# Optimization experiments

Hardware: AMD Instinct MI355X
Metric: run time of the kernel (lower is better)

The kernel has to match this reference:

```python
import jax, jax.numpy as jnp
import numpy as np

SR = 48000.0
STAB_EPS = 1e-3
BS = 32
N_FRAMES = 128
N_SAMPLES = 65536


def setup_inputs() -> dict:
    key = jax.random.key(0)
    ks = jax.random.split(key, 8)
    f0_hz = jax.random.uniform(ks[0], (BS,), minval=50.0, maxval=500.0)
    note_on_duration = jax.random.uniform(ks[1], (BS,), minval=0.3, maxval=1.0)
    phase = jax.random.uniform(ks[2], (BS,), minval=-np.pi, maxval=np.pi)
    logits = jax.random.normal(ks[3], (BS, N_FRAMES, 5))
    osc_shape = jax.random.uniform(ks[4], (BS,))
    osc_gain = jax.random.uniform(ks[5], (BS,), minval=0.5, maxval=1.0)
    dist_gain = jax.random.uniform(ks[6], (BS,), minval=1.0, maxval=4.0)
    learned_alpha = jax.random.uniform(ks[7], (BS,), minval=0.5, maxval=3.0)
    return dict(f0_hz=f0_hz, note_on_duration=note_on_duration, phase=phase,
                logits=logits, osc_shape=osc_shape, osc_gain=osc_gain,
                dist_gain=dist_gain, learned_alpha=learned_alpha,
                n_samples=N_SAMPLES)


def lin_interp_dim1(x, n_out):
    """Linear interpolation along dim 1 with align_corners=True. x: (bs, n_in, c)."""
    n_in = x.shape[1]
    pos = jnp.linspace(0.0, n_in - 1.0, n_out)
    i0 = jnp.floor(pos).astype(jnp.int32)
    i1 = jnp.minimum(i0 + 1, n_in - 1)
    frac = (pos - i0.astype(x.dtype))[None, :, None]
    return x[:, i0] * (1.0 - frac) + x[:, i1] * frac


def square_saw_vco(f0_hz, osc_shape, n_samples, phase):
    """torchsynth-style square/saw morph oscillator. f0_hz, osc_shape, phase: (bs,)."""
    f0 = f0_hz[:, None]                                   # (bs, 1)
    inc = jnp.broadcast_to(f0 / SR, (f0.shape[0], n_samples))
    arg = 2.0 * jnp.pi * jnp.cumsum(inc, axis=1) + phase[:, None]
    partials = 12000.0 / (f0 * jnp.log10(f0))
    square = jnp.tanh(jnp.pi * partials * jnp.sin(arg) / 2.0)
    s = osc_shape[:, None]
    return (1.0 - s / 2.0) * square * (1.0 + s * jnp.cos(arg / 2.0))


def exp_decay_env(alpha, note_on_duration, n_samples):
    t = jnp.arange(n_samples, dtype=jnp.float32) / SR     # (n,)
    ramp = jnp.clip(1.0 - t[None, :] / note_on_duration[:, None], STAB_EPS, 1.0)
    env = ramp ** alpha[:, None]
    return jnp.where(t[None, :] <= note_on_duration[:, None], env, 0.0)


def logits_to_a_coeff_triangle(a_logits):
    """Map 2 logits to a stable biquad denominator (a1, a2) inside the stability triangle."""
    stab = 1.0 - STAB_EPS
    a1 = 2.0 * jnp.tanh(a_logits[..., 0]) * stab
    a1_abs = jnp.abs(a1)
    a2 = ((2.0 - a1_abs) * jnp.tanh(a_logits[..., 1]) * stab + a1_abs) / 2.0
    return jnp.stack([a1, a2], axis=-1)


def sample_wise_lpc(x, a):
    """Time-varying all-pole order-2: y[t] = x[t] - a1[t]*y[t-1] - a2[t]*y[t-2].
    x: (bs, n), a: (bs, n, 2). Sequential lax.scan over time."""
    def step(carry, inp):
        y1, y2 = carry
        xt, a1, a2 = inp
        y = xt - a1 * y1 - a2 * y2
        return (y, y1), y
    z = jnp.zeros(x.shape[0], dtype=x.dtype)
    xs = (x.T, a[..., 0].T, a[..., 1].T)                  # time-major
    _, ys = jax.lax.scan(step, (z, z), xs)
    return ys.T


def time_varying_fir(x, b):
    """y[t] = b0[t]*x[t] + b1[t]*x[t-1] + b2[t]*x[t-2], zero initial state."""
    x1 = jnp.pad(x, ((0, 0), (1, 0)))[:, :-1]
    x2 = jnp.pad(x, ((0, 0), (2, 0)))[:, :-2]
    return b[..., 0] * x + b[..., 1] * x1 + b[..., 2] * x2


def reference(f0_hz, note_on_duration, phase, logits, osc_shape, osc_gain,
              dist_gain, learned_alpha, n_samples):
    # --- oscillator + envelope ---
    dry = square_saw_vco(f0_hz, osc_shape, n_samples, phase)
    dry = dry * osc_gain[:, None]
    envelope = exp_decay_env(learned_alpha, note_on_duration, n_samples)
    dry = dry * envelope
    # --- coefficients (interp_logits=False: map to coeffs at frame rate, then upsample) ---
    a_coeff = logits_to_a_coeff_triangle(logits[..., :2])   # (bs, n_frames, 2)
    b_coeff = logits[..., 2:]                                # (bs, n_frames, 3)
    a_coeff = lin_interp_dim1(a_coeff, n_samples)            # (bs, n, 2)
    b_coeff = lin_interp_dim1(b_coeff, n_samples)            # (bs, n, 3)
    # --- time-varying biquad: all-pole recursion then FIR ---
    y_a = sample_wise_lpc(dry, a_coeff)
    y_ab = time_varying_fir(y_a, b_coeff)
    # --- distortion ---
    wet = jnp.tanh(y_ab * dist_gain[:, None])
    a0 = jnp.ones_like(a_coeff[:, :, 0])
    a_coeff3 = jnp.stack([a0, a_coeff[:, :, 0], a_coeff[:, :, 1]], axis=2)
    return (dry, wet, envelope, y_ab, a_coeff3, b_coeff, y_a)
```

## Files before the change

### kernel.cpp

```cpp
#include <hip/hip_runtime.h>
#include <cmath>

#define DI __device__ __forceinline__

constexpr int BS = 32;
constexpr int NS = 65536;
constexpr int NF = 128;
constexpr int S  = 4;
constexpr int TB = 256;
constexpr int SAMP = TB * S;
constexpr int NC = NS / SAMP;
constexpr size_t U = (size_t)BS * NS;
constexpr double PI_D = 3.14159265358979323846;
constexpr float STAB = 0.999f;

struct M6 { float a, b, c, d, u, v; };

DI M6 comp(const M6& R, const M6& L) {
    M6 o;
    o.a = fmaf(R.a, L.a, R.b * L.c);
    o.b = fmaf(R.a, L.b, R.b * L.d);
    o.c = fmaf(R.c, L.a, R.d * L.c);
    o.d = fmaf(R.c, L.b, R.d * L.d);
    o.u = fmaf(R.a, L.u, fmaf(R.b, L.v, R.u));
    o.v = fmaf(R.c, L.u, fmaf(R.d, L.v, R.v));
    return o;
}

DI void stepL(M6& A, float a1, float a2, float x) {
    float na = fmaf(-a1, A.a, -a2 * A.c);
    float nb = fmaf(-a1, A.b, -a2 * A.d);
    float nu = fmaf(-a1, A.u, fmaf(-a2, A.v, x));
    A.c = A.a; A.d = A.b; A.v = A.u;
    A.a = na;  A.b = nb;  A.u = nu;
}

DI void wave_scan6(M6& s, int lane) {
    #pragma unroll
    for (int d = 1; d < 64; d <<= 1) {
        M6 o;
        o.a = __shfl_up(s.a, d, 64); o.b = __shfl_up(s.b, d, 64);
        o.c = __shfl_up(s.c, d, 64); o.d = __shfl_up(s.d, d, 64);
        o.u = __shfl_up(s.u, d, 64); o.v = __shfl_up(s.v, d, 64);
        M6 t = comp(s, o);
        bool p = lane >= d;
        s.a = p ? t.a : s.a; s.b = p ? t.b : s.b; s.c = p ? t.c : s.c;
        s.d = p ? t.d : s.d; s.u = p ? t.u : s.u; s.v = p ? t.v : s.v;
    }
}

DI M6 ld6(const float* p) { M6 m; m.a=p[0]; m.b=p[1]; m.c=p[2]; m.d=p[3]; m.u=p[4]; m.v=p[5]; return m; }
DI void st6(float* p, const M6& m) { p[0]=m.a; p[1]=m.b; p[2]=m.c; p[3]=m.d; p[4]=m.u; p[5]=m.v; }

DI void ipos(int t, int& i0, int& i1, float& fr) {
    double pos = (double)t * (127.0 / 65535.0);
    int p0 = (int)pos;
    i0 = p0;
    i1 = (p0 + 1 > 127) ? 127 : p0 + 1;
    fr = (float)(pos - (double)p0);
}

DI float fast_tanh(float x) {
    float e = __expf(2.0f * x);
    return 1.0f - 2.0f / (e + 1.0f);
}

DI void stage_frames(const float* __restrict__ logits, int b, int F, int tid,
                     float (*sfa)[2], float (*sfb)[3]) {
    if (tid < 4) {
        int fidx = F + tid; if (fidx > 127) fidx = 127;
        const float* L = logits + (size_t)(b * NF + fidx) * 5;
        float a1 = 2.0f * tanhf(L[0]) * STAB;
        float aa = fabsf(a1);
        float a2 = ((2.0f - aa) * tanhf(L[1]) * STAB + aa) * 0.5f;
        sfa[tid][0] = a1; sfa[tid][1] = a2;
        sfb[tid][0] = L[2]; sfb[tid][1] = L[3]; sfb[tid][2] = L[4];
    }
}

DI void interp4(int t0, int F, const float (*sfa)[2], const float (*sfb)[3],
                float* a1v, float* a2v, float* b0v, float* b1v, float* b2v) {
    #pragma unroll
    for (int k = 0; k < S; k++) {
        int i0, i1; float fr;
        ipos(t0 + k, i0, i1, fr);
        float w0 = 1.0f - fr;
        int l0 = i0 - F, l1 = i1 - F;
        a1v[k] = sfa[l0][0] * w0 + sfa[l1][0] * fr;
        a2v[k] = sfa[l0][1] * w0 + sfa[l1][1] * fr;
        b0v[k] = sfb[l0][0] * w0 + sfb[l1][0] * fr;
        b1v[k] = sfb[l0][1] * w0 + sfb[l1][1] * fr;
        b2v[k] = sfb[l0][2] * w0 + sfb[l1][2] * fr;
    }
}

__global__ __launch_bounds__(TB) void k_osc(
    const float* __restrict__ f0_hz, const float* __restrict__ note_dur,
    const float* __restrict__ phase, const float* __restrict__ logits,
    const float* __restrict__ osc_shape, const float* __restrict__ osc_gain,
    const float* __restrict__ alpha,
    float* __restrict__ ws_chunk, float* __restrict__ out) {
    __shared__ float sfa[4][2], sfb[4][3], wt[4][6];
    const int bid = blockIdx.x;
    const int b = bid / NC, c = bid % NC;
    const int tid = threadIdx.x;
    const int t0 = c * SAMP + tid * S;
    const size_t g0 = (size_t)b * NS + t0;
    const int F = (int)((double)(c * SAMP) * (127.0 / 65535.0));

    stage_frames(logits, b, F, tid, sfa, sfb);

    const float f0 = f0_hz[b];
    const float ph = phase[b];
    const float sh = osc_shape[b];
    const float gn = osc_gain[b];
    const float dur = note_dur[b];
    const float al = alpha[b];
    const double inc = (double)f0 / 48000.0;
    const float partials = 12000.0f / (f0 * __log10f(f0));

    const double cum0 = (double)(t0 + 1) * inc;
    const double uu0 = cum0 - 2.0 * floor(cum0 * 0.5);
    const float theta0 = (float)(PI_D * uu0 + 0.5 * (double)ph);
    const float dth = (float)(PI_D * inc);

    float x[S], env4[S];
    #pragma unroll
    for (int k = 0; k < S; k++) {
        int t = t0 + k;
        float theta = theta0 + (float)k * dth;
        float sn, cs;
        __sincosf(theta, &sn, &cs);
        float sq = fast_tanh(1.57079632679f * partials * (2.0f * sn * cs));
        float dry0 = (1.0f - 0.5f * sh) * sq * (1.0f + sh * cs);
        float tsec = (float)t * (1.0f / 48000.0f);
        float env = 0.0f;
        if (tsec <= dur) {
            float ramp = 1.0f - tsec / dur;
            ramp = ramp < 0.001f ? 0.001f : (ramp > 1.0f ? 1.0f : ramp);
            env = __expf(al * __logf(ramp));
        }
        env4[k] = env;
        x[k] = dry0 * gn * env;
    }
    __syncthreads();

    float a1v[S], a2v[S], b0v[S], b1v[S], b2v[S];
    interp4(t0, F, sfa, sfb, a1v, a2v, b0v, b1v, b2v);

    *(float4*)&out[g0]         = make_float4(x[0], x[1], x[2], x[3]);
    *(float4*)&out[2 * U + g0] = make_float4(env4[0], env4[1], env4[2], env4[3]);
    float* a3 = out + 4 * U + g0 * 3;
    *(float4*)&a3[0] = make_float4(1.0f, a1v[0], a2v[0], 1.0f);
    *(float4*)&a3[4] = make_float4(a1v[1], a2v[1], 1.0f, a1v[2]);
    *(float4*)&a3[8] = make_float4(a2v[2], 1.0f, a1v[3], a2v[3]);
    float* bc = out + 7 * U + g0 * 3;
    *(float4*)&bc[0] = make_float4(b0v[0], b1v[0], b2v[0], b0v[1]);
    *(float4*)&bc[4] = make_float4(b1v[1], b2v[1], b0v[2], b1v[2]);
    *(float4*)&bc[8] = make_float4(b2v[2], b0v[3], b1v[3], b2v[3]);

    M6 A; A.a = -a1v[0]; A.b = -a2v[0]; A.c = 1.0f; A.d = 0.0f; A.u = x[0]; A.v = 0.0f;
    #pragma unroll
    for (int k = 1; k < S; k++) stepL(A, a1v[k], a2v[k], x[k]);

    const int lane = tid & 63, w = tid >> 6;
    wave_scan6(A, lane);
    if (lane == 63) st6(wt[w], A);
    __syncthreads();
    if (tid == TB - 1) {
        M6 p = ld6(wt[0]);
        p = comp(ld6(wt[1]), p);
        p = comp(ld6(wt[2]), p);
        M6 tot = comp(A, p);
        st6(ws_chunk + ((size_t)b * NC + c) * 6, tot);
    }
}

__global__ __launch_bounds__(TB) void k_iir(
    const float* __restrict__ logits, const float* __restrict__ dist_gain,
    const float* __restrict__ ws_chunk, float* __restrict__ out) {
    __shared__ float sfa[4][2], sfb[4][3], wt[4][6], sv[NC][2];
    const int bid = blockIdx.x;
    const int b = bid / NC, c = bid % NC;
    const int tid = threadIdx.x;
    const int t0 = c * SAMP + tid * S;
    const size_t g0 = (size_t)b * NS + t0;
    const int F = (int)((double)(c * SAMP) * (127.0 / 65535.0));

    stage_frames(logits, b, F, tid, sfa, sfb);

    if (tid < NC) {
        M6 cs = ld6(ws_chunk + ((size_t)b * NC + tid) * 6);
        wave_scan6(cs, tid);
        sv[tid][0] = cs.u; sv[tid][1] = cs.v;
    }

    float4 xv = *(const float4*)&out[g0];
    float x[S] = {xv.x, xv.y, xv.z, xv.w};

    __syncthreads();
    const float s0 = c ? sv[c - 1][0] : 0.0f;
    const float s1 = c ? sv[c - 1][1] : 0.0f;

    float a1v[S], a2v[S], b0v[S], b1v[S], b2v[S];
    interp4(t0, F, sfa, sfb, a1v, a2v, b0v, b1v, b2v);

    M6 A; A.a = -a1v[0]; A.b = -a2v[0]; A.c = 1.0f; A.d = 0.0f; A.u = x[0]; A.v = 0.0f;
    #pragma unroll
    for (int k = 1; k < S; k++) stepL(A, a1v[k], a2v[k], x[k]);

    const int lane = tid & 63, w = tid >> 6;
    wave_scan6(A, lane);
    if (lane == 63) st6(wt[w], A);
    __syncthreads();

    M6 P; P.a = 1.f; P.b = 0.f; P.c = 0.f; P.d = 1.f; P.u = 0.f; P.v = 0.f;
    for (int i = 0; i < w; i++) P = comp(ld6(wt[i]), P);
    M6 prev;
    prev.a = __shfl_up(A.a, 1, 64); prev.b = __shfl_up(A.b, 1, 64);
    prev.c = __shfl_up(A.c, 1, 64); prev.d = __shfl_up(A.d, 1, 64);
    prev.u = __shfl_up(A.u, 1, 64); prev.v = __shfl_up(A.v, 1, 64);
    M6 E = (lane == 0) ? P : comp(prev, P);

    float y1 = fmaf(E.a, s0, fmaf(E.b, s1, E.u));
    float y2 = fmaf(E.c, s0, fmaf(E.d, s1, E.v));
    const float ys0 = y1, ys1 = y2;

    float y[S];
    #pragma unroll
    for (int k = 0; k < S; k++) {
        y[k] = fmaf(-a1v[k], y1, fmaf(-a2v[k], y2, x[k]));
        y2 = y1; y1 = y[k];
    }

    const float dg = dist_gain[b];
    float yab[S], wet[S];
    #pragma unroll
    for (int k = 0; k < S; k++) {
        float ym1 = (k >= 1) ? y[k - 1] : ys0;
        float ym2 = (k >= 2) ? y[k - 2] : ((k == 1) ? ys0 : ys1);
        yab[k] = b0v[k] * y[k] + b1v[k] * ym1 + b2v[k] * ym2;
        wet[k] = fast_tanh(yab[k] * dg);
    }

    *(float4*)&out[U + g0]      = make_float4(wet[0], wet[1], wet[2], wet[3]);
    *(float4*)&out[3 * U + g0]  = make_float4(yab[0], yab[1], yab[2], yab[3]);
    *(float4*)&out[10 * U + g0] = make_float4(y[0], y[1], y[2], y[3]);
}

extern "C" void kernel_launch(void* const* d_in, const int* in_sizes, int n_in,
                              void* d_out, int out_size, void* d_ws, size_t ws_size,
                              hipStream_t stream) {
    const float* f0   = (const float*)d_in[0];
    const float* dur  = (const float*)d_in[1];
    const float* ph   = (const float*)d_in[2];
    const float* lg   = (const float*)d_in[3];
    const float* shp  = (const float*)d_in[4];
    const float* gn   = (const float*)d_in[5];
    const float* dist = (const float*)d_in[6];
    const float* alp  = (const float*)d_in[7];
    float* out = (float*)d_out;
    float* ws_chunk = (float*)d_ws;

    k_osc<<<BS * NC, TB, 0, stream>>>(f0, dur, ph, lg, shp, gn, alp, ws_chunk, out);
    k_iir<<<BS * NC, TB, 0, stream>>>(lg, dist, ws_chunk, out);
}
```

Measured before the change: 130.6 us.

## Fuse oscillator and IIR kernels with decoupled look-back chunk scan

Merges the two-pass oscillator and IIR kernels into one kernel that keeps the dry signal and coefficients in registers. Blocks take a dynamic ticket to order chunks, publish their chunk transfer matrix with a release flag, and wait on predecessor flags before scanning them to get the carry-in state. This removes the second kernel's re-read of dry samples, its frame staging and coefficient re-interpolation, and one launch. In exchange it adds a tiny clear kernel, spin-waiting on global flags, and a bounded-guard loop that could silently produce wrong carries if a predecessor never arrives.

```diff
diff --git a/kernel.cpp b/kernel.cpp
--- a/kernel.cpp
+++ b/kernel.cpp
@@ -10,9 +10,14 @@
 constexpr int TB = 256;
 constexpr int SAMP = TB * S;
 constexpr int NC = NS / SAMP;
+constexpr int NBLK = BS * NC;
 constexpr size_t U = (size_t)BS * NS;
 constexpr double PI_D = 3.14159265358979323846;
 constexpr float STAB = 0.999f;
+
+__device__ unsigned int g_flags[NBLK];
+__device__ unsigned int g_tick;
+__device__ float        g_chunk[NBLK * 6];
 
 struct M6 { float a, b, c, d, u, v; };
 
@@ -94,16 +99,27 @@
     }
 }
 
-__global__ __launch_bounds__(TB) void k_osc(
+__global__ __launch_bounds__(TB) void k_clear() {
+    int i = blockIdx.x * TB + threadIdx.x;
+    if (i < NBLK) g_flags[i] = 0u;
+    if (i == 0) g_tick = 0u;
+}
+
+__global__ __launch_bounds__(TB) void k_fused(
     const float* __restrict__ f0_hz, const float* __restrict__ note_dur,
     const float* __restrict__ phase, const float* __restrict__ logits,
     const float* __restrict__ osc_shape, const float* __restrict__ osc_gain,
-    const float* __restrict__ alpha,
-    float* __restrict__ ws_chunk, float* __restrict__ out) {
-    __shared__ float sfa[4][2], sfb[4][3], wt[4][6];
-    const int bid = blockIdx.x;
-    const int b = bid / NC, c = bid % NC;
+    const float* __restrict__ dist_gain, const float* __restrict__ alpha,
+    float* __restrict__ out) {
+    __shared__ float sfa[4][2], sfb[4][3], wt[4][6], sIn[2];
+    __shared__ int s_v;
     const int tid = threadIdx.x;
+
+    if (tid == 0) s_v = (int)atomicAdd(&g_tick, 1u);
+    __syncthreads();
+    const int v = s_v;
+    const int b = v & (BS - 1);
+    const int c = v >> 5;
     const int t0 = c * SAMP + tid * S;
     const size_t g0 = (size_t)b * NS + t0;
     const int F = (int)((double)(c * SAMP) * (127.0 / 65535.0));
@@ -116,6 +132,7 @@
     const float gn = osc_gain[b];
     const float dur = note_dur[b];
     const float al = alpha[b];
+    const float dg = dist_gain[b];
     const double inc = (double)f0 / 48000.0;
     const float partials = 12000.0f / (f0 * __log10f(f0));
 
@@ -167,52 +184,46 @@
     wave_scan6(A, lane);
     if (lane == 63) st6(wt[w], A);
     __syncthreads();
+
     if (tid == TB - 1) {
         M6 p = ld6(wt[0]);
         p = comp(ld6(wt[1]), p);
         p = comp(ld6(wt[2]), p);
         M6 tot = comp(A, p);
-        st6(ws_chunk + ((size_t)b * NC + c) * 6, tot);
-    }
-}
-
-__global__ __launch_bounds__(TB) void k_iir(
-    const float* __restrict__ logits, const float* __restrict__ dist_gain,
-    const float* __restrict__ ws_chunk, float* __restrict__ out) {
-    __shared__ float sfa[4][2], sfb[4][3], wt[4][6], sv[NC][2];
-    const int bid = blockIdx.x;
-    const int b = bid / NC, c = bid % NC;
-    const int tid = threadIdx.x;
-    const int t0 = c * SAMP + tid * S;
-    const size_t g0 = (size_t)b * NS + t0;
-    const int F = (int)((double)(c * SAMP) * (127.0 / 65535.0));
-
-    stage_frames(logits, b, F, tid, sfa, sfb);
-
-    if (tid < NC) {
-        M6 cs = ld6(ws_chunk + ((size_t)b * NC + tid) * 6);
-        wave_scan6(cs, tid);
-        sv[tid][0] = cs.u; sv[tid][1] = cs.v;
-    }
-
-    float4 xv = *(const float4*)&out[g0];
-    float x[S] = {xv.x, xv.y, xv.z, xv.w};
-
-    __syncthreads();
-    const float s0 = c ? sv[c - 1][0] : 0.0f;
-    const float s1 = c ? sv[c - 1][1] : 0.0f;
-
-    float a1v[S], a2v[S], b0v[S], b1v[S], b2v[S];
-    interp4(t0, F, sfa, sfb, a1v, a2v, b0v, b1v, b2v);
-
-    M6 A; A.a = -a1v[0]; A.b = -a2v[0]; A.c = 1.0f; A.d = 0.0f; A.u = x[0]; A.v = 0.0f;
-    #pragma unroll
-    for (int k = 1; k < S; k++) stepL(A, a1v[k], a2v[k], x[k]);
-
-    const int lane = tid & 63, w = tid >> 6;
-    wave_scan6(A, lane);
-    if (lane == 63) st6(wt[w], A);
-    __syncthreads();
+        float* wp = g_chunk + (size_t)(b * NC + c) * 6;
+        __hip_atomic_store(wp + 0, tot.a, __ATOMIC_RELAXED, __HIP_MEMORY_SCOPE_AGENT);
+        __hip_atomic_store(wp + 1, tot.b, __ATOMIC_RELAXED, __HIP_MEMORY_SCOPE_AGENT);
+        __hip_atomic_store(wp + 2, tot.c, __ATOMIC_RELAXED, __HIP_MEMORY_SCOPE_AGENT);
+        __hip_atomic_store(wp + 3, tot.d, __ATOMIC_RELAXED, __HIP_MEMORY_SCOPE_AGENT);
+        __hip_atomic_store(wp + 4, tot.u, __ATOMIC_RELAXED, __HIP_MEMORY_SCOPE_AGENT);
+        __hip_atomic_store(wp + 5, tot.v, __ATOMIC_RELAXED, __HIP_MEMORY_SCOPE_AGENT);
+        __hip_atomic_store(&g_flags[b * NC + c], 1u, __ATOMIC_RELEASE, __HIP_MEMORY_SCOPE_AGENT);
+    }
+
+    if (tid < 64) {
+        M6 L; L.a = 1.f; L.b = 0.f; L.c = 0.f; L.d = 1.f; L.u = 0.f; L.v = 0.f;
+        if (tid < c) {
+            const unsigned int* fp = &g_flags[b * NC + tid];
+            int guard = 0;
+            while (__hip_atomic_load(fp, __ATOMIC_ACQUIRE, __HIP_MEMORY_SCOPE_AGENT) == 0u) {
+                __builtin_amdgcn_s_sleep(2);
+                if (++guard > (1 << 20)) break;
+            }
+            const float* wp = g_chunk + (size_t)(b * NC + tid) * 6;
+            L.a = __hip_atomic_load(wp + 0, __ATOMIC_RELAXED, __HIP_MEMORY_SCOPE_AGENT);
+            L.b = __hip_atomic_load(wp + 1, __ATOMIC_RELAXED, __HIP_MEMORY_SCOPE_AGENT);
+            L.c = __hip_atomic_load(wp + 2, __ATOMIC_RELAXED, __HIP_MEMORY_SCOPE_AGENT);
+            L.d = __hip_atomic_load(wp + 3, __ATOMIC_RELAXED, __HIP_MEMORY_SCOPE_AGENT);
+            L.u = __hip_atomic_load(wp + 4, __ATOMIC_RELAXED, __HIP_MEMORY_SCOPE_AGENT);
+            L.v = __hip_atomic_load(wp + 5, __ATOMIC_RELAXED, __HIP_MEMORY_SCOPE_AGENT);
+        }
+        wave_scan6(L, tid);
+        if (tid == 63) { sIn[0] = L.u; sIn[1] = L.v; }
+    }
+    __syncthreads();
+
+    const float s0 = sIn[0];
+    const float s1 = sIn[1];
 
     M6 P; P.a = 1.f; P.b = 0.f; P.c = 0.f; P.d = 1.f; P.u = 0.f; P.v = 0.f;
     for (int i = 0; i < w; i++) P = comp(ld6(wt[i]), P);
@@ -233,7 +244,6 @@
         y2 = y1; y1 = y[k];
     }
 
-    const float dg = dist_gain[b];
     float yab[S], wet[S];
     #pragma unroll
     for (int k = 0; k < S; k++) {
@@ -260,8 +270,7 @@
     const float* dist = (const float*)d_in[6];
     const float* alp  = (const float*)d_in[7];
     float* out = (float*)d_out;
-    float* ws_chunk = (float*)d_ws;
-
-    k_osc<<<BS * NC, TB, 0, stream>>>(f0, dur, ph, lg, shp, gn, alp, ws_chunk, out);
-    k_iir<<<BS * NC, TB, 0, stream>>>(lg, dist, ws_chunk, out);
-}
+
+    k_clear<<<(NBLK + TB - 1) / TB, TB, 0, stream>>>();
+    k_fused<<<NBLK, TB, 0, stream>>>(f0, dur, ph, lg, shp, gn, dist, alp, out);
+}
```

After: 321.0 us. +145.7%, slower.
